# Kernel tuning notes

Hardware: AMD Instinct MI355X
Metric: run time of the kernel (lower is better)

Reference implementation:

```python
import jax, jax.numpy as jnp
import numpy as np

B, S, H, K, V = 1024, 50, 128, 4, 100000
ROUTING_TIMES = 3

def _squash(c):
    # c: [B,K,1,H]
    cap_norm = jnp.sum(jnp.square(c), -1, keepdims=True)
    scalar_factor = cap_norm / (1.0 + cap_norm) / jnp.sqrt(cap_norm + 1e-9)
    return scalar_factor * c

def setup_inputs() -> dict:
    key = jax.random.key(0)
    k1, k2, k3, k4, k5, k6 = jax.random.split(key, 6)
    item_seq = jax.random.randint(k1, (B, S), 0, V)
    mask = jax.random.randint(k2, (B, S), 0, 2).astype(jnp.float32)
    item = jax.random.randint(k3, (B, 1), 0, V)
    emb = jax.random.normal(k4, (V, H), dtype=jnp.float32) * 0.02
    W = jax.random.normal(k5, (H, H), dtype=jnp.float32) * (1.0 / np.sqrt(H))
    # bilinear_type==0 -> capsule routing logits initialized with randn
    capsule_weight0 = jax.random.normal(k6, (B, K, S), dtype=jnp.float32)
    return {"item_seq": item_seq, "mask": mask, "item": item,
            "emb": emb, "W": W, "capsule_weight0": capsule_weight0}

def reference(item_seq, mask, item, emb, W, capsule_weight0):
    # padding_idx=0: lookups see a zeroed row 0 (and get no grad there),
    # but calculate_loss uses the raw weight matrix.
    emb_lookup = emb.at[0].set(0.0)
    seq_emb = emb_lookup[item_seq]          # [B,S,H]
    item_e = emb_lookup[item[:, 0]]         # [B,H]  (squeeze(1))

    # CapsuleNetwork, bilinear_type==0: Linear(H,H,no bias) then repeat_interleave along hidden
    h = seq_emb @ W.T                        # [B,S,H]
    hat = jnp.repeat(h, K, axis=2)           # [B,S,H*K] (repeat_interleave semantics)
    hat = hat.reshape(B, S, K, H).transpose(0, 2, 1, 3)  # [B,K,S,H]
    hat_iter = jax.lax.stop_gradient(hat)    # stop_grad=True (detach)

    atten_mask = jnp.broadcast_to(mask[:, None, :], (B, K, S))
    cw = capsule_weight0
    cap = None
    for i in range(ROUTING_TIMES):
        # torch F.softmax with no dim on a 3-D tensor uses dim=0 (batch axis) -- faithful
        sw = jax.nn.softmax(cw, axis=0)
        sw = jnp.where(atten_mask == 0, 0.0, sw)[:, :, None, :]  # [B,K,1,S]
        src = hat_iter if i < ROUTING_TIMES - 1 else hat
        cap = _squash(sw @ src)                                   # [B,K,1,H]
        if i < ROUTING_TIMES - 1:
            delta = (hat_iter @ jnp.swapaxes(cap, 3, 2)).reshape(B, K, S)
            cw = cw + delta

    user_emb = cap.reshape(B, K, H)          # multi_interest_emb

    # hard readout: pick interest with max dot against target item
    cos = jnp.einsum('bkh,bh->bk', user_emb, item_e)
    k_index = jnp.argmax(cos, axis=1)        # [B]
    best = jnp.take_along_axis(user_emb, k_index[:, None, None], axis=1)[:, 0]  # [B,H]

    # cross-entropy over all items (raw embedding weight)
    scores = best @ emb.T                    # [B,V]
    logp = jax.nn.log_softmax(scores, axis=-1)
    loss = -jnp.mean(jnp.take_along_axis(logp, item, axis=1))
    return user_emb, loss
```

## Files before the change

### kernel.cpp

```cpp
#include <hip/hip_runtime.h>
#include <math.h>

#define BB 1024
#define SS 50
#define SSP 51
#define HH 128
#define KK 4
#define VV 100000
#define NVT 782
#define NVT8 784
#define VPAD (NVT8*128)
#define KS (KK*SS)
#define NHM 400
#define NPAD_LAST 96.0f

typedef __attribute__((ext_vector_type(8))) short bf16x8;
typedef __attribute__((ext_vector_type(4))) float f32x4;

__device__ __forceinline__ ushort f2bf(float x) {
  unsigned u = __float_as_uint(x);
  unsigned r = u + 0x7FFF + ((u >> 16) & 1);
  return (ushort)(r >> 16);
}
__device__ __forceinline__ float bf2f(ushort u) {
  return __uint_as_float(((unsigned)u) << 16);
}
__device__ __forceinline__ bf16x8 cvt8(float4 a, float4 b) {
  bf16x8 r;
  r[0] = (short)f2bf(a.x); r[1] = (short)f2bf(a.y);
  r[2] = (short)f2bf(a.z); r[3] = (short)f2bf(a.w);
  r[4] = (short)f2bf(b.x); r[5] = (short)f2bf(b.y);
  r[6] = (short)f2bf(b.z); r[7] = (short)f2bf(b.w);
  return r;
}

__global__ __launch_bounds__(256) void k_conv(const float* __restrict__ emb,
                                              ushort* __restrict__ embb) {
  size_t i = ((size_t)blockIdx.x * 256 + threadIdx.x) * 4;
  ushort4 o;
  if (i < (size_t)VV * HH) {
    float4 v = *(const float4*)&emb[i];
    o = make_ushort4(f2bf(v.x), f2bf(v.y), f2bf(v.z), f2bf(v.w));
  } else {
    o = make_ushort4(0, 0, 0, 0);
  }
  *(ushort4*)&embb[i] = o;
}

__global__ __launch_bounds__(256) void k_pre(const float* __restrict__ emb,
                                             const float* __restrict__ cw0,
                                             float* __restrict__ cm,
                                             float* __restrict__ s1,
                                             float* __restrict__ s2,
                                             float* __restrict__ accum,
                                             const int* __restrict__ item_seq,
                                             const float* __restrict__ W,
                                             ushort* __restrict__ hb16) {
  const int t = threadIdx.x;
  if (blockIdx.x < NHM) {
    __shared__ __align__(16) ushort sWf[32 * 512];
    const int w = t >> 6;
    const int lane = t & 63;
    const int lr = lane & 15;
    const int lq = lane >> 4;
    const int m0 = blockIdx.x * 128;

#pragma unroll
    for (int it = 0; it < 8; ++it) {
      int pos = t + it * 256;
      int ch = pos >> 6, l = pos & 63;
      int n = (ch & 7) * 16 + (l & 15);
      int k0 = (ch >> 3) * 32 + (l >> 4) * 8;
      float4 a = *(const float4*)&W[n * HH + k0];
      float4 b = *(const float4*)&W[n * HH + k0 + 4];
      *(bf16x8*)&sWf[ch * 512 + l * 8] = cvt8(a, b);
    }

    bf16x8 af[4][2];
#pragma unroll
    for (int vv = 0; vv < 2; ++vv) {
      int m = m0 + w * 32 + vv * 16 + lr;
      int idx = item_seq[m];
#pragma unroll
      for (int ks = 0; ks < 4; ++ks) {
        if (idx != 0) {
          float4 a = *(const float4*)&emb[(size_t)idx * HH + ks * 32 + lq * 8];
          float4 b = *(const float4*)&emb[(size_t)idx * HH + ks * 32 + lq * 8 + 4];
          af[ks][vv] = cvt8(a, b);
        } else {
          af[ks][vv] = (bf16x8){0, 0, 0, 0, 0, 0, 0, 0};
        }
      }
    }
    __syncthreads();

    f32x4 acc[8][2];
#pragma unroll
    for (int nt = 0; nt < 8; ++nt)
#pragma unroll
      for (int vv = 0; vv < 2; ++vv) acc[nt][vv] = (f32x4){0.f, 0.f, 0.f, 0.f};

#pragma unroll
    for (int ks = 0; ks < 4; ++ks) {
      bf16x8 bw[8];
#pragma unroll
      for (int nt = 0; nt < 8; ++nt)
        bw[nt] = *(const bf16x8*)&sWf[(ks * 8 + nt) * 512 + lane * 8];
#pragma unroll
      for (int nt = 0; nt < 8; ++nt)
#pragma unroll
        for (int vv = 0; vv < 2; ++vv)
          acc[nt][vv] = __builtin_amdgcn_mfma_f32_16x16x32_bf16(af[ks][vv], bw[nt], acc[nt][vv], 0, 0, 0);
    }

#pragma unroll
    for (int nt = 0; nt < 8; ++nt)
#pragma unroll
      for (int vv = 0; vv < 2; ++vv)
#pragma unroll
        for (int r = 0; r < 4; ++r) {
          int m = m0 + w * 32 + vv * 16 + lq * 4 + r;
          hb16[(size_t)m * HH + nt * 16 + lr] = f2bf(acc[nt][vv][r]);
        }
  } else {
    __shared__ float red[256];
    const int c = blockIdx.x - NHM;
    if (t < 8) s1[t * KS + c] = 0.f;
    if (t >= 8 && t < 16) s2[(t - 8) * KS + c] = 0.f;
    if (c < 4) accum[c * 256 + t] = 0.f;
    float s = 0.f;
    for (int b = t; b < BB; b += 256) s += __expf(cw0[(size_t)b * KS + c]);
    red[t] = s;
    __syncthreads();
    for (int o = 128; o > 0; o >>= 1) {
      if (t < o) red[t] += red[t + o];
      __syncthreads();
    }
    if (t == 0) cm[c] = red[0];
  }
}

__global__ __launch_bounds__(256) void k_route(const float* __restrict__ cwsrc,
                                               float* __restrict__ cwdst,
                                               const ushort* __restrict__ hb16,
                                               const float* __restrict__ csum,
                                               int nslots,
                                               const float* __restrict__ mask,
                                               int last,
                                               float* __restrict__ out_ue,
                                               const float* __restrict__ emb,
                                               const int* __restrict__ item,
                                               ushort* __restrict__ bestb,
                                               float* __restrict__ csnext,
                                               float* __restrict__ si) {
  __shared__ ushort shT[128 * SSP];
  __shared__ float swl[KS];
  __shared__ float c32p[256];
  __shared__ float c32[128];
  __shared__ float csq[128];
  __shared__ float ie4r[32];
  __shared__ float ie4z[32];
  __shared__ float fac[4];
  __shared__ float cosk[4];
  __shared__ float cosr[4];
  __shared__ int kb;
  const int t = threadIdx.x;
  const int b = blockIdx.x;

  for (int p = t; p < (SS * HH) / 4; p += 256) {
    int flat = 4 * p;
    int s = flat >> 7, col = flat & 127;
    ushort4 v = *(const ushort4*)&hb16[(size_t)b * SS * HH + flat];
    shT[(col + 0) * SSP + s] = v.x;
    shT[(col + 1) * SSP + s] = v.y;
    shT[(col + 2) * SSP + s] = v.z;
    shT[(col + 3) * SSP + s] = v.w;
  }
  if (t < KS) {
    float den = 0.f;
    for (int g2 = 0; g2 < nslots; ++g2) den += csum[g2 * KS + t];
    float v = __expf(cwsrc[(size_t)b * KS + t]) / den;
    if (mask[b * SS + (t % SS)] == 0.0f) v = 0.0f;
    swl[t] = v;
  }
  __syncthreads();

  {
    int col = t & 127;
    int half = t >> 7;
    int k = col >> 5;
    float acc = 0.f;
    const float* swk = &swl[k * SS + half * 25];
    const ushort* hc = &shT[col * SSP + half * 25];
    for (int s = 0; s < 25; ++s) acc += swk[s] * bf2f(hc[s]);
    c32p[t] = acc;
  }
  __syncthreads();
  if (t < 128) c32[t] = c32p[t] + c32p[t + 128];
  __syncthreads();
  if (t < 4) {
    float nrm = 0.f;
#pragma unroll
    for (int j = 0; j < 32; ++j) { float c = c32[32 * t + j]; nrm += c * c; }
    nrm *= 4.0f;
    fac[t] = nrm / (1.0f + nrm) / sqrtf(nrm + 1e-9f);
  }
  __syncthreads();
  if (t < 128) csq[t] = c32[t] * fac[t >> 5];
  __syncthreads();

  if (!last) {
    if (t < KS) {
      int k = t / SS, s = t % SS;
      const float* cq = &csq[32 * k];
      float d = 0.f;
#pragma unroll
      for (int j = 0; j < 32; ++j) d += bf2f(shT[(32 * k + j) * SSP + s]) * cq[j];
      float nv = cwsrc[(size_t)b * KS + t] + 4.0f * d;
      cwdst[(size_t)b * KS + t] = nv;
      atomicAdd(&csnext[(b & 7) * KS + t], __expf(nv));
    }
  } else {
    for (int hh = t; hh < 512; hh += 256) {
      int k = hh >> 7, r = (hh & 127) >> 2;
      out_ue[(size_t)b * 512 + hh] = csq[32 * k + r];
    }
    if (t < 32) {
      int idx = item[b];
      const float* e = emb + (size_t)idx * HH + 4 * t;
      float v = e[0] + e[1] + e[2] + e[3];
      ie4r[t] = v;
      ie4z[t] = (idx == 0) ? 0.f : v;
    }
    __syncthreads();
    if (t < 4) {
      float cz = 0.f, cr = 0.f;
#pragma unroll
      for (int j = 0; j < 32; ++j) {
        cz += csq[32 * t + j] * ie4z[j];
        cr += csq[32 * t + j] * ie4r[j];
      }
      cosk[t] = cz; cosr[t] = cr;
    }
    __syncthreads();
    if (t == 0) {
      int kbest = 0; float bv = cosk[0];
#pragma unroll
      for (int k = 1; k < 4; ++k) if (cosk[k] > bv) { bv = cosk[k]; kbest = k; }
      kb = kbest;
      si[b] = cosr[kbest];
    }
    __syncthreads();
    if (t < 128) bestb[(size_t)b * HH + t] = f2bf(csq[32 * kb + (t >> 2)]);
  }
}

__global__ __launch_bounds__(256) void k_score_mfma(const ushort* __restrict__ bestb,
                                                    const ushort* __restrict__ embb,
                                                    float* __restrict__ accum) {
  const int lin = blockIdx.x;
  const int xcd = lin & 7;
  const int g = lin >> 3;
  const int bt8 = g & 7;
  const int vt = xcd * (NVT8 / 8) + (g >> 3);
  if (vt >= NVT) return;

  __shared__ __align__(16) ushort sB[32 * 512];
  __shared__ float ssm[128][4];
  const int t = threadIdx.x;
  const int w = t >> 6;
  const int lane = t & 63;
  const int lr = lane & 15;
  const int lq = lane >> 4;
  const int b0 = bt8 * 128;
  const int v0 = vt * 128 + w * 32;

  bf16x8 af[4][2];
#pragma unroll
  for (int ks = 0; ks < 4; ++ks)
#pragma unroll
    for (int vv = 0; vv < 2; ++vv)
      af[ks][vv] = *(const bf16x8*)&embb[(size_t)(v0 + vv * 16 + lr) * HH + ks * 32 + lq * 8];

#pragma unroll
  for (int it = 0; it < 8; ++it) {
    int pos = t + it * 256;
    int ch = pos >> 6;
    int l = pos & 63;
    int ks = ch >> 3, bt = ch & 7;
    *(bf16x8*)&sB[ch * 512 + l * 8] =
        *(const bf16x8*)&bestb[(size_t)(b0 + bt * 16 + (l & 15)) * HH + ks * 32 + (l >> 4) * 8];
  }

  f32x4 acc[8][2];
#pragma unroll
  for (int bt = 0; bt < 8; ++bt)
#pragma unroll
    for (int vv = 0; vv < 2; ++vv) acc[bt][vv] = (f32x4){0.f, 0.f, 0.f, 0.f};

  __syncthreads();

  bf16x8 bcur[8];
#pragma unroll
  for (int bt = 0; bt < 8; ++bt)
    bcur[bt] = *(const bf16x8*)&sB[bt * 512 + lane * 8];

#pragma unroll
  for (int ks = 0; ks < 4; ++ks) {
    bf16x8 bnxt[8];
    if (ks < 3) {
#pragma unroll
      for (int bt = 0; bt < 8; ++bt)
        bnxt[bt] = *(const bf16x8*)&sB[((ks + 1) * 8 + bt) * 512 + lane * 8];
    }
#pragma unroll
    for (int bt = 0; bt < 8; ++bt)
#pragma unroll
      for (int vv = 0; vv < 2; ++vv)
        acc[bt][vv] = __builtin_amdgcn_mfma_f32_16x16x32_bf16(af[ks][vv], bcur[bt], acc[bt][vv], 0, 0, 0);
    if (ks < 3) {
#pragma unroll
      for (int bt = 0; bt < 8; ++bt) bcur[bt] = bnxt[bt];
    }
  }

#pragma unroll
  for (int bt = 0; bt < 8; ++bt) {
    float s = 0.f;
#pragma unroll
    for (int vv = 0; vv < 2; ++vv)
#pragma unroll
      for (int r = 0; r < 4; ++r) s += __expf(acc[bt][vv][r]);
    s += __shfl_xor(s, 16);
    s += __shfl_xor(s, 32);
    if (lq == 0) ssm[bt * 16 + lr][w] = s;
  }
  __syncthreads();
  if (t < 128) {
    float s = ssm[t][0] + ssm[t][1] + ssm[t][2] + ssm[t][3];
    atomicAdd(&accum[b0 + t], s);
  }
}

__global__ __launch_bounds__(256) void k_loss(const float* __restrict__ accum,
                                              const float* __restrict__ si,
                                              float* __restrict__ outloss) {
  __shared__ float red[256];
  const int t = threadIdx.x;
  float s = 0.f;
  for (int b = t; b < BB; b += 256)
    s += logf(accum[b] - NPAD_LAST) - si[b];
  red[t] = s;
  __syncthreads();
  for (int o = 128; o > 0; o >>= 1) {
    if (t < o) red[t] += red[t + o];
    __syncthreads();
  }
  if (t == 0) outloss[0] = red[0] / (float)BB;
}

extern "C" void kernel_launch(void* const* d_in, const int* in_sizes, int n_in,
                              void* d_out, int out_size, void* d_ws, size_t ws_size,
                              hipStream_t stream) {
  const int*   item_seq = (const int*)d_in[0];
  const float* mask     = (const float*)d_in[1];
  const int*   item     = (const int*)d_in[2];
  const float* emb      = (const float*)d_in[3];
  const float* W        = (const float*)d_in[4];
  const float* cw0      = (const float*)d_in[5];
  float* out = (float*)d_out;
  float* outloss = out + (size_t)BB * KK * HH;

  float* ws = (float*)d_ws;
  float* cm    = ws;
  float* s1    = cm + 256;
  float* s2    = s1 + 8 * KS;
  float* si    = s2 + 8 * KS;
  float* accum = si + BB;
  float* cw    = accum + BB;
  ushort* hb16  = (ushort*)(cw + (size_t)BB * KS);
  ushort* embb  = hb16 + (size_t)BB * SS * HH;
  ushort* bestb = embb + (size_t)VPAD * HH;

  k_pre<<<dim3(NHM + KS), 256, 0, stream>>>(emb, cw0, cm, s1, s2, accum,
                                            item_seq, W, hb16);
  k_conv<<<dim3((VPAD * HH) / 1024), 256, 0, stream>>>(emb, embb);

  k_route<<<dim3(BB), 256, 0, stream>>>(cw0, cw, hb16, cm, 1, mask, 0, out, emb, item, bestb, s1, si);
  k_route<<<dim3(BB), 256, 0, stream>>>(cw, cw, hb16, s1, 8, mask, 0, out, emb, item, bestb, s2, si);
  k_route<<<dim3(BB), 256, 0, stream>>>(cw, cw, hb16, s2, 8, mask, 1, out, emb, item, bestb, s1, si);

  k_score_mfma<<<dim3(NVT8 * 8), 256, 0, stream>>>(bestb, embb, accum);
  k_loss<<<dim3(1), 256, 0, stream>>>(accum, si, outloss);
}
```

Measured before the change: 200.4 us.

## Fuse bf16 embedding conversion into pre kernel and process two vocab tiles per score block

The separate fp32-to-bf16 embedding conversion kernel is merged into k_pre as extra grid-stride blocks, removing one launch and letting the conversion run alongside the W projection. The score kernel now handles two 128-row vocab tiles per block, reusing the staged best-interest tile in shared memory and halving the grid. The best-interest vector is pre-scaled by log2(e) so the hardware exp2 can be used, and the count of padded rows subtracted in the loss is updated to the new padding layout (352 padded rows). Costs are more registers per thread for the doubled A fragments, and the hardcoded tile arithmetic (xcd*98) has to cover exactly the padded vocab range.

```diff
diff --git a/kernel.cpp b/kernel.cpp
--- a/kernel.cpp
+++ b/kernel.cpp
@@ -12,7 +12,10 @@
 #define VPAD (NVT8*128)
 #define KS (KK*SS)
 #define NHM 400
-#define NPAD_LAST 96.0f
+#define NPAD_ALL 352.0f
+#define CONVB 2048
+#define LOG2E 1.44269504f
+#define SGRID ((NVT8/2)*8)
 
 typedef __attribute__((ext_vector_type(8))) short bf16x8;
 typedef __attribute__((ext_vector_type(4))) float f32x4;
@@ -32,19 +35,6 @@
   r[4] = (short)f2bf(b.x); r[5] = (short)f2bf(b.y);
   r[6] = (short)f2bf(b.z); r[7] = (short)f2bf(b.w);
   return r;
-}
-
-__global__ __launch_bounds__(256) void k_conv(const float* __restrict__ emb,
-                                              ushort* __restrict__ embb) {
-  size_t i = ((size_t)blockIdx.x * 256 + threadIdx.x) * 4;
-  ushort4 o;
-  if (i < (size_t)VV * HH) {
-    float4 v = *(const float4*)&emb[i];
-    o = make_ushort4(f2bf(v.x), f2bf(v.y), f2bf(v.z), f2bf(v.w));
-  } else {
-    o = make_ushort4(0, 0, 0, 0);
-  }
-  *(ushort4*)&embb[i] = o;
 }
 
 __global__ __launch_bounds__(256) void k_pre(const float* __restrict__ emb,
@@ -55,7 +45,8 @@
                                              float* __restrict__ accum,
                                              const int* __restrict__ item_seq,
                                              const float* __restrict__ W,
-                                             ushort* __restrict__ hb16) {
+                                             ushort* __restrict__ hb16,
+                                             ushort* __restrict__ embb) {
   const int t = threadIdx.x;
   if (blockIdx.x < NHM) {
     __shared__ __align__(16) ushort sWf[32 * 512];
@@ -122,7 +113,7 @@
           int m = m0 + w * 32 + vv * 16 + lq * 4 + r;
           hb16[(size_t)m * HH + nt * 16 + lr] = f2bf(acc[nt][vv][r]);
         }
-  } else {
+  } else if (blockIdx.x < NHM + KS) {
     __shared__ float red[256];
     const int c = blockIdx.x - NHM;
     if (t < 8) s1[t * KS + c] = 0.f;
@@ -137,6 +128,19 @@
       __syncthreads();
     }
     if (t == 0) cm[c] = red[0];
+  } else {
+    const size_t stride = (size_t)CONVB * 256 * 4;
+    for (size_t i = ((size_t)(blockIdx.x - NHM - KS) * 256 + t) * 4;
+         i < (size_t)VPAD * HH; i += stride) {
+      ushort4 o;
+      if (i < (size_t)VV * HH) {
+        float4 v = *(const float4*)&emb[i];
+        o = make_ushort4(f2bf(v.x), f2bf(v.y), f2bf(v.z), f2bf(v.w));
+      } else {
+        o = make_ushort4(0, 0, 0, 0);
+      }
+      *(ushort4*)&embb[i] = o;
+    }
   }
 }
 
@@ -251,7 +255,7 @@
       si[b] = cosr[kbest];
     }
     __syncthreads();
-    if (t < 128) bestb[(size_t)b * HH + t] = f2bf(csq[32 * kb + (t >> 2)]);
+    if (t < 128) bestb[(size_t)b * HH + t] = f2bf(csq[32 * kb + (t >> 2)] * LOG2E);
   }
 }
 
@@ -262,8 +266,7 @@
   const int xcd = lin & 7;
   const int g = lin >> 3;
   const int bt8 = g & 7;
-  const int vt = xcd * (NVT8 / 8) + (g >> 3);
-  if (vt >= NVT) return;
+  const int vt0 = xcd * 98 + (g >> 3) * 2;
 
   __shared__ __align__(16) ushort sB[32 * 512];
   __shared__ float ssm[128][4];
@@ -273,14 +276,17 @@
   const int lr = lane & 15;
   const int lq = lane >> 4;
   const int b0 = bt8 * 128;
-  const int v0 = vt * 128 + w * 32;
-
-  bf16x8 af[4][2];
-#pragma unroll
-  for (int ks = 0; ks < 4; ++ks)
+
+  bf16x8 af[2][4][2];
+#pragma unroll
+  for (int i = 0; i < 2; ++i) {
+    const int v0 = (vt0 + i) * 128 + w * 32;
 #pragma unroll
     for (int vv = 0; vv < 2; ++vv)
-      af[ks][vv] = *(const bf16x8*)&embb[(size_t)(v0 + vv * 16 + lr) * HH + ks * 32 + lq * 8];
+#pragma unroll
+      for (int ks = 0; ks < 4; ++ks)
+        af[i][ks][vv] = *(const bf16x8*)&embb[(size_t)(v0 + vv * 16 + lr) * HH + ks * 32 + lq * 8];
+  }
 
 #pragma unroll
   for (int it = 0; it < 8; ++it) {
@@ -291,46 +297,55 @@
     *(bf16x8*)&sB[ch * 512 + l * 8] =
         *(const bf16x8*)&bestb[(size_t)(b0 + bt * 16 + (l & 15)) * HH + ks * 32 + (l >> 4) * 8];
   }
-
-  f32x4 acc[8][2];
-#pragma unroll
-  for (int bt = 0; bt < 8; ++bt)
-#pragma unroll
-    for (int vv = 0; vv < 2; ++vv) acc[bt][vv] = (f32x4){0.f, 0.f, 0.f, 0.f};
-
-  __syncthreads();
-
-  bf16x8 bcur[8];
-#pragma unroll
-  for (int bt = 0; bt < 8; ++bt)
-    bcur[bt] = *(const bf16x8*)&sB[bt * 512 + lane * 8];
-
-#pragma unroll
-  for (int ks = 0; ks < 4; ++ks) {
-    bf16x8 bnxt[8];
-    if (ks < 3) {
+  __builtin_amdgcn_sched_barrier(0);
+
+  float sacc[8];
+#pragma unroll
+  for (int bt = 0; bt < 8; ++bt) sacc[bt] = 0.f;
+
+  __syncthreads();
+
+#pragma unroll
+  for (int i = 0; i < 2; ++i) {
+    f32x4 acc[8][2];
+#pragma unroll
+    for (int bt = 0; bt < 8; ++bt)
+#pragma unroll
+      for (int vv = 0; vv < 2; ++vv) acc[bt][vv] = (f32x4){0.f, 0.f, 0.f, 0.f};
+
+#pragma unroll
+    for (int ks = 0; ks < 4; ++ks) {
+      bf16x8 bw[8];
 #pragma unroll
       for (int bt = 0; bt < 8; ++bt)
-        bnxt[bt] = *(const bf16x8*)&sB[((ks + 1) * 8 + bt) * 512 + lane * 8];
-    }
-#pragma unroll
-    for (int bt = 0; bt < 8; ++bt)
+        bw[bt] = *(const bf16x8*)&sB[(ks * 8 + bt) * 512 + lane * 8];
+#pragma unroll
+      for (int bt = 0; bt < 8; ++bt)
+#pragma unroll
+        for (int vv = 0; vv < 2; ++vv)
+          acc[bt][vv] = __builtin_amdgcn_mfma_f32_16x16x32_bf16(af[i][ks][vv], bw[bt], acc[bt][vv], 0, 0, 0);
+    }
+
+#pragma unroll
+    for (int bt = 0; bt < 8; ++bt) {
+      float e[8];
 #pragma unroll
       for (int vv = 0; vv < 2; ++vv)
-        acc[bt][vv] = __builtin_amdgcn_mfma_f32_16x16x32_bf16(af[ks][vv], bcur[bt], acc[bt][vv], 0, 0, 0);
-    if (ks < 3) {
-#pragma unroll
-      for (int bt = 0; bt < 8; ++bt) bcur[bt] = bnxt[bt];
+#pragma unroll
+        for (int r = 0; r < 4; ++r)
+          e[vv * 4 + r] = __builtin_amdgcn_exp2f(acc[bt][vv][r]);
+#pragma unroll
+      for (int o = 4; o > 0; o >>= 1)
+#pragma unroll
+        for (int j = 0; j < 8; ++j)
+          if (j < o) e[j] += e[j + o];
+      sacc[bt] += e[0];
     }
   }
 
 #pragma unroll
   for (int bt = 0; bt < 8; ++bt) {
-    float s = 0.f;
-#pragma unroll
-    for (int vv = 0; vv < 2; ++vv)
-#pragma unroll
-      for (int r = 0; r < 4; ++r) s += __expf(acc[bt][vv][r]);
+    float s = sacc[bt];
     s += __shfl_xor(s, 16);
     s += __shfl_xor(s, 32);
     if (lq == 0) ssm[bt * 16 + lr][w] = s;
@@ -349,7 +364,7 @@
   const int t = threadIdx.x;
   float s = 0.f;
   for (int b = t; b < BB; b += 256)
-    s += logf(accum[b] - NPAD_LAST) - si[b];
+    s += logf(accum[b] - NPAD_ALL) - si[b];
   red[t] = s;
   __syncthreads();
   for (int o = 128; o > 0; o >>= 1) {
@@ -382,14 +397,13 @@
   ushort* embb  = hb16 + (size_t)BB * SS * HH;
   ushort* bestb = embb + (size_t)VPAD * HH;
 
-  k_pre<<<dim3(NHM + KS), 256, 0, stream>>>(emb, cw0, cm, s1, s2, accum,
-                                            item_seq, W, hb16);
-  k_conv<<<dim3((VPAD * HH) / 1024), 256, 0, stream>>>(emb, embb);
+  k_pre<<<dim3(NHM + KS + CONVB), 256, 0, stream>>>(emb, cw0, cm, s1, s2, accum,
+                                                    item_seq, W, hb16, embb);
 
   k_route<<<dim3(BB), 256, 0, stream>>>(cw0, cw, hb16, cm, 1, mask, 0, out, emb, item, bestb, s1, si);
   k_route<<<dim3(BB), 256, 0, stream>>>(cw, cw, hb16, s1, 8, mask, 0, out, emb, item, bestb, s2, si);
   k_route<<<dim3(BB), 256, 0, stream>>>(cw, cw, hb16, s2, 8, mask, 1, out, emb, item, bestb, s1, si);
 
-  k_score_mfma<<<dim3(NVT8 * 8), 256, 0, stream>>>(bestb, embb, accum);
+  k_score_mfma<<<dim3(SGRID), 256, 0, stream>>>(bestb, embb, accum);
   k_loss<<<dim3(1), 256, 0, stream>>>(accum, si, outloss);
 }
```

After: 223.9 us. +11.7%, slower.
